# Performance work log

Hardware: AMD Instinct MI355X
Metric: run time of the kernel (lower is better)

The kernel has to match this reference:

```python
import jax, jax.numpy as jnp
import numpy as np

P = 1  # padding (= kernel_size // 2 for 3x3 convs), matches init_kwargs


def _rot(a, k):
    # torch x.rot90(k, dims=(-2, -1)) equivalent
    return jnp.rot90(a, k, axes=(-2, -1))


def _tl(p, top, lft):
    # interpolated top-left corner for equatorial faces (no shared pixel)
    ret = jnp.zeros(top.shape[:-2] + (p, p), top.dtype)
    ret = ret.at[..., -1, -1].set(0.5 * top[..., -1, 0] + 0.5 * lft[..., 0, -1])
    for i in range(1, p):
        ret = ret.at[..., -i - 1, -i:].set(top[..., -i - 1, :i])
        ret = ret.at[..., -i:, -i - 1].set(lft[..., :i, -i - 1])
        ret = ret.at[..., -i - 1, -i - 1].set(0.5 * top[..., -i - 1, 0] + 0.5 * lft[..., 0, -i - 1])
    return ret


def _br(p, b, r):
    # interpolated bottom-right corner for equatorial faces
    ret = jnp.zeros(b.shape[:-2] + (p, p), b.dtype)
    ret = ret.at[..., 0, 0].set(0.5 * b[..., 0, -1] + 0.5 * r[..., -1, 0])
    for i in range(1, p):
        ret = ret.at[..., :i, i].set(r[..., -i:, i])
        ret = ret.at[..., i, :i].set(b[..., i, -i:])
        ret = ret.at[..., i, i].set(0.5 * b[..., i, -1] + 0.5 * r[..., -1, i])
    return ret


def _pn(p, c, t, tl, lft, bl, b, br, rgt, tr):
    # north polar face: top neighbour rotated +90deg, top-left +180deg
    c = jnp.concatenate([_rot(t, 1)[..., -p:, :], c, b[..., :p, :]], axis=-2)
    left = jnp.concatenate([_rot(tl, 2)[..., -p:, -p:], _rot(lft, -1)[..., -p:], bl[..., :p, -p:]], axis=-2)
    right = jnp.concatenate([tr[..., -p:, :p], rgt[..., :p], br[..., :p, :p]], axis=-2)
    return jnp.concatenate([left, c, right], axis=-1)


def _pe(p, c, t, tl, lft, bl, b, br, rgt, tr):
    # equatorial face: no rotations
    c = jnp.concatenate([t[..., -p:, :], c, b[..., :p, :]], axis=-2)
    left = jnp.concatenate([tl[..., -p:, -p:], lft[..., -p:], bl[..., :p, -p:]], axis=-2)
    right = jnp.concatenate([tr[..., -p:, :p], rgt[..., :p], br[..., :p, :p]], axis=-2)
    return jnp.concatenate([left, c, right], axis=-1)


def _ps(p, c, t, tl, lft, bl, b, br, rgt, tr):
    # south polar face: bottom +90deg, right -90deg, bottom-right +180deg
    c = jnp.concatenate([t[..., -p:, :], c, _rot(b, 1)[..., :p, :]], axis=-2)
    left = jnp.concatenate([tl[..., -p:, -p:], lft[..., -p:], bl[..., :p, -p:]], axis=-2)
    right = jnp.concatenate([tr[..., -p:, :p], _rot(rgt, -1)[..., :p], _rot(br, 2)[..., :p, :p]], axis=-2)
    return jnp.concatenate([left, c, right], axis=-1)


def _healpix_pad(x, p):
    B12, C, n, _ = x.shape
    x5 = x.reshape(B12 // 12, 12, C, n, n)  # (B, 12, C, n, n)
    f = [x5[:, i] for i in range(12)]
    pads = [
        _pn(p, f[0], f[1], f[2], f[3], f[3], f[4], f[8], f[5], f[1]),
        _pn(p, f[1], f[2], f[3], f[0], f[0], f[5], f[9], f[6], f[2]),
        _pn(p, f[2], f[3], f[0], f[1], f[1], f[6], f[10], f[7], f[3]),
        _pn(p, f[3], f[0], f[1], f[2], f[2], f[7], f[11], f[4], f[0]),
        _pe(p, f[4], f[0], _tl(p, f[0], f[3]), f[3], f[7], f[11], _br(p, f[11], f[8]), f[8], f[5]),
        _pe(p, f[5], f[1], _tl(p, f[1], f[0]), f[0], f[4], f[8], _br(p, f[8], f[9]), f[9], f[6]),
        _pe(p, f[6], f[2], _tl(p, f[2], f[1]), f[1], f[5], f[9], _br(p, f[9], f[10]), f[10], f[7]),
        _pe(p, f[7], f[3], _tl(p, f[3], f[2]), f[2], f[6], f[10], _br(p, f[10], f[11]), f[11], f[4]),
        _ps(p, f[8], f[5], f[0], f[4], f[11], f[11], f[10], f[9], f[9]),
        _ps(p, f[9], f[6], f[1], f[5], f[8], f[8], f[11], f[10], f[10]),
        _ps(p, f[10], f[7], f[2], f[6], f[9], f[9], f[8], f[11], f[11]),
        _ps(p, f[11], f[4], f[3], f[7], f[10], f[10], f[9], f[8], f[8]),
    ]
    out = jnp.stack(pads, axis=1)  # (B, 12, C, n+2p, n+2p)
    return out.reshape(B12, C, n + 2 * p, n + 2 * p)


def setup_inputs() -> dict:
    key = jax.random.key(0)
    x = jax.random.normal(key, (24, 128, 128, 128), dtype=jnp.float32)
    return {"x": x}


def reference(x):
    return _healpix_pad(x, P)
```

## Files before the change

### kernel.cpp

```cpp
#include <hip/hip_runtime.h>


#define NPLANE_OUT 16900

__device__ __forceinline__ float hp_face(const float* __restrict__ in, size_t baseoff,
                                         int q, int i, int j) {
  return in[baseoff + ((size_t)q << 21) + (i << 7) + j];
}

__device__ __forceinline__ float hp_val(const float* __restrict__ in, size_t baseoff,
                                        int type, int m, int face, int r, int col) {
  const int L = 127;
  if (r == 0) {
    if (col == 0) {
      if (type == 0) return hp_face(in, baseoff, (m + 2) & 3, 0, 0);
      if (type == 1) return 0.5f * (hp_face(in, baseoff, m, L, 0) +
                                    hp_face(in, baseoff, (m + 3) & 3, 0, L));
      return hp_face(in, baseoff, m, L, L);
    }
    if (col == 129) {
      if (type == 0) return hp_face(in, baseoff, (m + 1) & 3, L, 0);
      if (type == 1) return hp_face(in, baseoff, 4 + ((m + 1) & 3), L, 0);
      return hp_face(in, baseoff, 8 + ((m + 1) & 3), L, 0);
    }
    int j = col - 1;
    if (type == 0) return hp_face(in, baseoff, (m + 1) & 3, j, 0);
    if (type == 1) return hp_face(in, baseoff, m, L, j);
    return hp_face(in, baseoff, 4 + ((m + 1) & 3), L, j);
  }
  if (r == 129) {
    if (col == 0) {
      if (type == 0) return hp_face(in, baseoff, (m + 3) & 3, 0, L);
      if (type == 1) return hp_face(in, baseoff, 4 + ((m + 3) & 3), 0, L);
      return hp_face(in, baseoff, 8 + ((m + 3) & 3), 0, L);
    }
    if (col == 129) {
      if (type == 0) return hp_face(in, baseoff, 8 + m, 0, 0);
      if (type == 1) return 0.5f * (hp_face(in, baseoff, 8 + ((m + 3) & 3), 0, L) +
                                    hp_face(in, baseoff, 8 + m, L, 0));
      return hp_face(in, baseoff, 8 + ((m + 2) & 3), L, L);
    }
    int j = col - 1;
    if (type == 0) return hp_face(in, baseoff, 4 + m, 0, j);
    if (type == 1) return hp_face(in, baseoff, 8 + ((m + 3) & 3), 0, j);
    return hp_face(in, baseoff, 8 + ((m + 3) & 3), j, L);
  }
  int i = r - 1;
  if (col == 0) {
    if (type == 0) return hp_face(in, baseoff, (m + 3) & 3, 0, i);
    if (type == 1) return hp_face(in, baseoff, (m + 3) & 3, i, L);
    return hp_face(in, baseoff, 4 + m, i, L);
  }
  if (type == 0) return hp_face(in, baseoff, 4 + ((m + 1) & 3), i, 0);
  if (type == 1) return hp_face(in, baseoff, 8 + m, i, 0);
  return hp_face(in, baseoff, 8 + ((m + 1) & 3), L, i);
}

typedef float f4v __attribute__((ext_vector_type(4)));
typedef f4v f4u __attribute__((aligned(4)));

__global__ __launch_bounds__(256) void CREDITHEALPix_90975997264316_kernel(
    const float* __restrict__ in, float* __restrict__ out) {
  int plane = blockIdx.y;
  int b12 = plane >> 7;
  int c = plane & 127;
  int batch = (b12 >= 12) ? 1 : 0;
  int face = b12 - batch * 12;
  int type = face >> 2;
  int m = face & 3;
  size_t baseoff = (((size_t)batch * 1536) + (size_t)c) << 14;
  size_t face_off = baseoff + ((size_t)face << 21);
  float* __restrict__ oplane = out + (size_t)plane * NPLANE_OUT;

  if (blockIdx.x < 4) {
    const float* __restrict__ src = in + face_off;
    int q0 = blockIdx.x * 1024 + threadIdx.x;
    f4v v0, v1, v2, v3;
    {
      int q = q0;
      v0 = __builtin_nontemporal_load((const f4v*)(src + (size_t)((q >> 5) << 7) + ((q & 31) << 2)));
      q = q0 + 256;
      v1 = __builtin_nontemporal_load((const f4v*)(src + (size_t)((q >> 5) << 7) + ((q & 31) << 2)));
      q = q0 + 512;
      v2 = __builtin_nontemporal_load((const f4v*)(src + (size_t)((q >> 5) << 7) + ((q & 31) << 2)));
      q = q0 + 768;
      v3 = __builtin_nontemporal_load((const f4v*)(src + (size_t)((q >> 5) << 7) + ((q & 31) << 2)));
    }
    {
      int q = q0;
      *(f4u*)(oplane + ((q >> 5) + 1) * 130 + 1 + ((q & 31) << 2)) = v0;
      q = q0 + 256;
      *(f4u*)(oplane + ((q >> 5) + 1) * 130 + 1 + ((q & 31) << 2)) = v1;
      q = q0 + 512;
      *(f4u*)(oplane + ((q >> 5) + 1) * 130 + 1 + ((q & 31) << 2)) = v2;
      q = q0 + 768;
      *(f4u*)(oplane + ((q >> 5) + 1) * 130 + 1 + ((q & 31) << 2)) = v3;
    }
  } else {
    for (int e = threadIdx.x; e < 516; e += 256) {
      int r, col;
      if (e < 130)      { r = 0;       col = e; }
      else if (e < 260) { r = 129;     col = e - 130; }
      else if (e < 388) { r = e - 259; col = 0; }
      else              { r = e - 387; col = 129; }
      oplane[r * 130 + col] = hp_val(in, baseoff, type, m, face, r, col);
    }
  }
}

extern "C" void kernel_launch(void* const* d_in, const int* in_sizes, int n_in,
                              void* d_out, int out_size, void* d_ws, size_t ws_size,
                              hipStream_t stream) {
  const float* in = (const float*)d_in[0];
  float* out = (float*)d_out;
  dim3 grid(5, 3072, 1);
  dim3 block(256, 1, 1);
  CREDITHEALPix_90975997264316_kernel<<<grid, block, 0, stream>>>(in, out);
}
```

Measured before the change: 372.4 us.

## Iterate over output plane with aligned float4 stores and merged border handling

Replaces the split into four interior blocks and one border block per plane with a single block per plane. That block walks the output plane in 16-byte-aligned float4 chunks, gathering the interior from the input with scalar loads and computing border elements inline. The aim is to make every output store an aligned vector store, since output rows of 130 floats made the old interior stores misaligned, and to drop the separate border block. In exchange, input reads become unaligned scalar loads without the nontemporal hint, each thread does integer division, and there are fewer, larger blocks.

```diff
diff --git a/kernel.cpp b/kernel.cpp
--- a/kernel.cpp
+++ b/kernel.cpp
@@ -57,11 +57,10 @@
 }
 
 typedef float f4v __attribute__((ext_vector_type(4)));
-typedef f4v f4u __attribute__((aligned(4)));
 
 __global__ __launch_bounds__(256) void CREDITHEALPix_90975997264316_kernel(
     const float* __restrict__ in, float* __restrict__ out) {
-  int plane = blockIdx.y;
+  int plane = blockIdx.x;
   int b12 = plane >> 7;
   int c = plane & 127;
   int batch = (b12 >= 12) ? 1 : 0;
@@ -69,42 +68,34 @@
   int type = face >> 2;
   int m = face & 3;
   size_t baseoff = (((size_t)batch * 1536) + (size_t)c) << 14;
-  size_t face_off = baseoff + ((size_t)face << 21);
+  const float* __restrict__ src = in + baseoff + ((size_t)face << 21);
   float* __restrict__ oplane = out + (size_t)plane * NPLANE_OUT;
 
-  if (blockIdx.x < 4) {
-    const float* __restrict__ src = in + face_off;
-    int q0 = blockIdx.x * 1024 + threadIdx.x;
-    f4v v0, v1, v2, v3;
-    {
-      int q = q0;
-      v0 = __builtin_nontemporal_load((const f4v*)(src + (size_t)((q >> 5) << 7) + ((q & 31) << 2)));
-      q = q0 + 256;
-      v1 = __builtin_nontemporal_load((const f4v*)(src + (size_t)((q >> 5) << 7) + ((q & 31) << 2)));
-      q = q0 + 512;
-      v2 = __builtin_nontemporal_load((const f4v*)(src + (size_t)((q >> 5) << 7) + ((q & 31) << 2)));
-      q = q0 + 768;
-      v3 = __builtin_nontemporal_load((const f4v*)(src + (size_t)((q >> 5) << 7) + ((q & 31) << 2)));
+  for (int t4 = threadIdx.x; t4 < 4225; t4 += 256) {
+    int e = t4 << 2;
+    int r = e / 130;
+    int col = e - r * 130;
+    f4v v;
+    if (r >= 1 && r <= 128 && col >= 1 && col <= 125) {
+      const float* __restrict__ p = src + ((r - 1) << 7) + (col - 1);
+      v[0] = p[0];
+      v[1] = p[1];
+      v[2] = p[2];
+      v[3] = p[3];
+    } else {
+      #pragma unroll
+      for (int k = 0; k < 4; ++k) {
+        int ek = e + k;
+        int rk = ek / 130;
+        int ck = ek - rk * 130;
+        if (rk == 0 || rk == 129 || ck == 0 || ck == 129) {
+          v[k] = hp_val(in, baseoff, type, m, face, rk, ck);
+        } else {
+          v[k] = src[((rk - 1) << 7) + (ck - 1)];
+        }
+      }
     }
-    {
-      int q = q0;
-      *(f4u*)(oplane + ((q >> 5) + 1) * 130 + 1 + ((q & 31) << 2)) = v0;
-      q = q0 + 256;
-      *(f4u*)(oplane + ((q >> 5) + 1) * 130 + 1 + ((q & 31) << 2)) = v1;
-      q = q0 + 512;
-      *(f4u*)(oplane + ((q >> 5) + 1) * 130 + 1 + ((q & 31) << 2)) = v2;
-      q = q0 + 768;
-      *(f4u*)(oplane + ((q >> 5) + 1) * 130 + 1 + ((q & 31) << 2)) = v3;
-    }
-  } else {
-    for (int e = threadIdx.x; e < 516; e += 256) {
-      int r, col;
-      if (e < 130)      { r = 0;       col = e; }
-      else if (e < 260) { r = 129;     col = e - 130; }
-      else if (e < 388) { r = e - 259; col = 0; }
-      else              { r = e - 387; col = 129; }
-      oplane[r * 130 + col] = hp_val(in, baseoff, type, m, face, r, col);
-    }
+    *(f4v*)(oplane + e) = v;
   }
 }
 
@@ -113,7 +104,7 @@
                               hipStream_t stream) {
   const float* in = (const float*)d_in[0];
   float* out = (float*)d_out;
-  dim3 grid(5, 3072, 1);
+  dim3 grid(3072, 1, 1);
   dim3 block(256, 1, 1);
   CREDITHEALPix_90975997264316_kernel<<<grid, block, 0, stream>>>(in, out);
 }
```

After: 379.6 us. No clear change (+1.9%).
